# Performance work log

Hardware: AMD Instinct MI355X
Metric: run time of the kernel (lower is better)

## Reference

```python
import jax, jax.numpy as jnp
import numpy as np

D_MODEL = 1024
NUM_HEADS = 16
HEAD_DIM = D_MODEL // NUM_HEADS


def setup_inputs() -> dict:
    key = jax.random.key(0)
    ks = jax.random.split(key, 6)
    B, S = 2, 2048
    s = 1.0 / np.sqrt(D_MODEL)
    return {
        "x": jax.random.normal(ks[0], (B, S, D_MODEL), dtype=jnp.float32),
        "Wq": jax.random.normal(ks[1], (D_MODEL, D_MODEL), dtype=jnp.float32) * s,
        "Wk": jax.random.normal(ks[2], (D_MODEL, D_MODEL), dtype=jnp.float32) * s,
        "Wv": jax.random.normal(ks[3], (D_MODEL, D_MODEL), dtype=jnp.float32) * s,
        "Wo": jax.random.normal(ks[4], (D_MODEL, D_MODEL), dtype=jnp.float32) * s,
        "bo": jax.random.normal(ks[5], (D_MODEL,), dtype=jnp.float32) * 0.01,
    }


def reference(x, Wq, Wk, Wv, Wo, bo):
    b, n, _ = x.shape
    # QKV projections (no bias, qkv_bias=False); weights applied as x @ W^T like nn.Linear
    q = (x @ Wq.T).reshape(b, n, NUM_HEADS, HEAD_DIM).transpose(0, 2, 1, 3)  # [b,h,n,d]
    k = (x @ Wk.T).reshape(b, n, NUM_HEADS, HEAD_DIM).transpose(0, 2, 1, 3)
    v = (x @ Wv.T).reshape(b, n, NUM_HEADS, HEAD_DIM).transpose(0, 2, 1, 3)
    scores = jnp.einsum("bhqd,bhkd->bhqk", q, k)
    causal = jnp.tril(jnp.ones((n, n), dtype=bool))  # keep where True
    scores = jnp.where(causal, scores, -jnp.inf)
    weights = jax.nn.softmax(scores / np.sqrt(HEAD_DIM), axis=-1)
    # dropout p=0.0 -> identity (eval semantics)
    ctx = jnp.einsum("bhqk,bhkd->bhqd", weights, v)
    ctx = ctx.transpose(0, 2, 1, 3).reshape(b, n, D_MODEL)
    return ctx @ Wo.T + bo
```

## Files before the change

### kernel.cpp

```cpp
#include <hip/hip_runtime.h>

#define D_MODEL 1024
#define NUM_HEADS 16
#define HEAD_DIM 64
#define BATCH 2
#define SEQ 2048
#define MTOT (BATCH * SEQ)

typedef __attribute__((ext_vector_type(8))) short bf16x8;
typedef __attribute__((ext_vector_type(4))) short s16x4;
typedef __attribute__((ext_vector_type(4))) float f32x4;
typedef unsigned short u16;
typedef unsigned long long u64;

__device__ __forceinline__ u16 f2bf(float f) {
    unsigned u = __float_as_uint(f);
    return (u16)((u + 0x7FFFu + ((u >> 16) & 1u)) >> 16);
}
__device__ __forceinline__ float bf2f(u16 v) {
    return __uint_as_float((unsigned)v << 16);
}

__device__ __forceinline__ unsigned cvt_pk_bf16(float lo, float hi) {
    unsigned r;
    asm volatile("v_cvt_pk_bf16_f32 %0, %1, %2" : "=v"(r) : "v"(lo), "v"(hi));
    return r;
}

#if __has_builtin(__builtin_amdgcn_exp2f)
#define EXP2(x) __builtin_amdgcn_exp2f(x)
#else
#define EXP2(x) exp2f(x)
#endif

#define GLOAD16(gp, lp) __builtin_amdgcn_global_load_lds(                      \
    (const __attribute__((address_space(1))) void*)(gp),                       \
    (__attribute__((address_space(3))) void*)(lp), 16, 0, 0)

__global__ __launch_bounds__(256)
void cast_all_kernel(const float* __restrict__ x,  const float* __restrict__ Wq,
                     const float* __restrict__ Wk, const float* __restrict__ Wv,
                     const float* __restrict__ Wo, u16* __restrict__ dst)
{
    const int i = blockIdx.x * 256 + threadIdx.x;
    const float* src;
    int j;
    if (i < 524288) { src = x; j = i; }
    else if (i < 917504) {
        const int k = i - 524288;
        const int z = k >> 17;
        src = (z == 0) ? Wq : (z == 1) ? Wk : Wv;
        j = k & 0x1FFFF;
    } else { src = Wo; j = i - 917504; }
    const float4* s = reinterpret_cast<const float4*>(src) + (size_t)j * 2;
    float4 a = s[0], b = s[1];
    u16 tmp[8] = {f2bf(a.x), f2bf(a.y), f2bf(a.z), f2bf(a.w),
                  f2bf(b.x), f2bf(b.y), f2bf(b.z), f2bf(b.w)};
    *reinterpret_cast<int4*>(dst + (size_t)i * 8) = *reinterpret_cast<int4*>(tmp);
}

__global__ __launch_bounds__(512, 4)
void gemm_qkv_kernel(const u16* __restrict__ A, const u16* __restrict__ B,
                     u16* __restrict__ Qo, u16* __restrict__ Ko, u16* __restrict__ Vt)
{
    __shared__ u16 Al[3][128 * 32];
    __shared__ u16 Bl[3][256 * 32];

    const int tid = threadIdx.x;
    const int l = tid & 63;
    const int w = tid >> 6;
    const int wm = w >> 2, wn = w & 3;
    const int lr = l & 15, lg = l >> 4;

    const int bid = blockIdx.x;
    const int swz = (bid & 7) * 48 + (bid >> 3);
    const int mb = swz / 12, nb = swz % 12;
    const int m0 = mb * 128, n0 = nb * 256;

    const int arow = tid >> 2;
    const int acol = ((tid & 3) ^ ((arow >> 1) & 3)) * 8;
    const int br1  = (512 + tid) >> 2;
    const int bcol1 = ((tid & 3) ^ ((br1 >> 1) & 3)) * 8;
    const int dst0 = tid * 8;
    const int dst1 = 4096 + tid * 8;
    const int rsw = (lr >> 1) & 3;

    f32x4 acc[4][4];
    #pragma unroll
    for (int i = 0; i < 4; ++i)
        #pragma unroll
        for (int j = 0; j < 4; ++j) acc[i][j] = (f32x4){0.f, 0.f, 0.f, 0.f};

    #pragma unroll
    for (int t = 0; t < 2; ++t) {
        const int k0 = t * 32;
        GLOAD16(A + (size_t)(m0 + arow) * D_MODEL + k0 + acol,  &Al[t][dst0]);
        GLOAD16(B + (size_t)(n0 + arow) * D_MODEL + k0 + acol,  &Bl[t][dst0]);
        GLOAD16(B + (size_t)(n0 + br1)  * D_MODEL + k0 + bcol1, &Bl[t][dst1]);
    }

    int cb = 0;
    for (int t = 0; t < 32; ++t) {
        if (t < 31) asm volatile("s_waitcnt vmcnt(3)" ::: "memory");
        else        asm volatile("s_waitcnt vmcnt(0)" ::: "memory");
        __builtin_amdgcn_s_barrier();

        if (t + 2 < 32) {
            const int sb = (cb >= 1) ? cb - 1 : cb + 2;
            const int k0 = (t + 2) * 32;
            GLOAD16(A + (size_t)(m0 + arow) * D_MODEL + k0 + acol,  &Al[sb][dst0]);
            GLOAD16(B + (size_t)(n0 + arow) * D_MODEL + k0 + acol,  &Bl[sb][dst0]);
            GLOAD16(B + (size_t)(n0 + br1)  * D_MODEL + k0 + bcol1, &Bl[sb][dst1]);
        }

        const u16* __restrict__ Ab = Al[cb];
        const u16* __restrict__ Bb = Bl[cb];
        bf16x8 af[4], bfr[4];
        #pragma unroll
        for (int i = 0; i < 4; ++i)
            af[i] = *reinterpret_cast<const bf16x8*>(
                &Ab[(wm * 64 + i * 16 + lr) * 32 + ((lg ^ rsw) * 8)]);
        #pragma unroll
        for (int j = 0; j < 4; ++j)
            bfr[j] = *reinterpret_cast<const bf16x8*>(
                &Bb[(wn * 64 + j * 16 + lr) * 32 + ((lg ^ rsw) * 8)]);

        __builtin_amdgcn_s_setprio(1);
        #pragma unroll
        for (int i = 0; i < 4; ++i)
            #pragma unroll
            for (int j = 0; j < 4; ++j)
                acc[i][j] = __builtin_amdgcn_mfma_f32_16x16x32_bf16(
                    af[i], bfr[j], acc[i][j], 0, 0, 0);
        __builtin_amdgcn_s_setprio(0);

        cb = (cb == 2) ? 0 : cb + 1;
    }

    const int z = (n0 >> 10);
    if (z < 2) {
        #pragma unroll
        for (int i = 0; i < 4; ++i) {
            #pragma unroll
            for (int r = 0; r < 4; ++r) {
                const int m = m0 + wm * 64 + i * 16 + lg * 4 + r;
                const int bb = m >> 11, s = m & (SEQ - 1);
                #pragma unroll
                for (int j = 0; j < 4; ++j) {
                    const int c = n0 + wn * 64 + j * 16 + lr;
                    const int cc = c & 1023, h = cc >> 6, d = cc & 63;
                    const size_t idx = ((size_t)(bb * NUM_HEADS + h) * SEQ + s) * 64 + d;
                    if (z == 0) Qo[idx] = f2bf(acc[i][j][r] * 0.18033688f);
                    else        Ko[idx] = f2bf(acc[i][j][r]);
                }
            }
        }
    } else {
        #pragma unroll
        for (int i = 0; i < 4; ++i) {
            const int mbase = m0 + wm * 64 + i * 16 + lg * 4;
            const int bb = mbase >> 11, s = mbase & (SEQ - 1);
            #pragma unroll
            for (int j = 0; j < 4; ++j) {
                const int c = n0 + wn * 64 + j * 16 + lr;
                const int cc = c & 1023, h = cc >> 6, d = cc & 63;
                u16 t4[4];
                #pragma unroll
                for (int r = 0; r < 4; ++r) t4[r] = f2bf(acc[i][j][r]);
                *reinterpret_cast<u64*>(
                    &Vt[((size_t)(bb * NUM_HEADS + h) * 64 + d) * SEQ + s]) =
                    *reinterpret_cast<u64*>(t4);
            }
        }
    }
}

__global__ __launch_bounds__(256, 3)
void gemm_out_kernel(const u16* __restrict__ A, const u16* __restrict__ B,
                     const float* __restrict__ bias, float* __restrict__ out)
{
    __shared__ u16 Al[3][128 * 32];
    __shared__ u16 Bl[3][128 * 32];

    const int tid = threadIdx.x;
    const int l = tid & 63;
    const int w = tid >> 6;
    const int wm = w >> 1, wn = w & 1;
    const int lr = l & 15, lg = l >> 4;

    const int bid = blockIdx.x;
    const int swz = (bid & 7) * 32 + (bid >> 3);
    const int mb = swz >> 3, nb = swz & 7;
    const int m0 = mb * 128, n0 = nb * 128;

    const int r0 = tid >> 2;
    const int c0 = ((tid & 3) ^ ((r0 >> 1) & 3)) * 8;
    const int r1 = 64 + (tid >> 2);
    const int c1 = ((tid & 3) ^ ((r1 >> 1) & 3)) * 8;
    const int dst0 = tid * 8;
    const int dst1 = 2048 + tid * 8;
    const int rsw = (lr >> 1) & 3;

    f32x4 acc[4][4];
    #pragma unroll
    for (int i = 0; i < 4; ++i)
        #pragma unroll
        for (int j = 0; j < 4; ++j) acc[i][j] = (f32x4){0.f, 0.f, 0.f, 0.f};

    #pragma unroll
    for (int t = 0; t < 2; ++t) {
        const int k0 = t * 32;
        GLOAD16(A + (size_t)(m0 + r0) * D_MODEL + k0 + c0, &Al[t][dst0]);
        GLOAD16(A + (size_t)(m0 + r1) * D_MODEL + k0 + c1, &Al[t][dst1]);
        GLOAD16(B + (size_t)(n0 + r0) * D_MODEL + k0 + c0, &Bl[t][dst0]);
        GLOAD16(B + (size_t)(n0 + r1) * D_MODEL + k0 + c1, &Bl[t][dst1]);
    }

    int cb = 0;
    for (int t = 0; t < 32; ++t) {
        if (t < 31) asm volatile("s_waitcnt vmcnt(4)" ::: "memory");
        else        asm volatile("s_waitcnt vmcnt(0)" ::: "memory");
        __builtin_amdgcn_s_barrier();

        if (t + 2 < 32) {
            const int sb = (cb >= 1) ? cb - 1 : cb + 2;
            const int k0 = (t + 2) * 32;
            GLOAD16(A + (size_t)(m0 + r0) * D_MODEL + k0 + c0, &Al[sb][dst0]);
            GLOAD16(A + (size_t)(m0 + r1) * D_MODEL + k0 + c1, &Al[sb][dst1]);
            GLOAD16(B + (size_t)(n0 + r0) * D_MODEL + k0 + c0, &Bl[sb][dst0]);
            GLOAD16(B + (size_t)(n0 + r1) * D_MODEL + k0 + c1, &Bl[sb][dst1]);
        }

        const u16* __restrict__ Ab = Al[cb];
        const u16* __restrict__ Bb = Bl[cb];
        bf16x8 af[4], bfr[4];
        #pragma unroll
        for (int i = 0; i < 4; ++i)
            af[i] = *reinterpret_cast<const bf16x8*>(
                &Ab[(wm * 64 + i * 16 + lr) * 32 + ((lg ^ rsw) * 8)]);
        #pragma unroll
        for (int j = 0; j < 4; ++j)
            bfr[j] = *reinterpret_cast<const bf16x8*>(
                &Bb[(wn * 64 + j * 16 + lr) * 32 + ((lg ^ rsw) * 8)]);

        __builtin_amdgcn_s_setprio(1);
        #pragma unroll
        for (int i = 0; i < 4; ++i)
            #pragma unroll
            for (int j = 0; j < 4; ++j)
                acc[i][j] = __builtin_amdgcn_mfma_f32_16x16x32_bf16(
                    af[i], bfr[j], acc[i][j], 0, 0, 0);
        __builtin_amdgcn_s_setprio(0);

        cb = (cb == 2) ? 0 : cb + 1;
    }

    #pragma unroll
    for (int i = 0; i < 4; ++i) {
        #pragma unroll
        for (int r = 0; r < 4; ++r) {
            const int m = m0 + wm * 64 + i * 16 + lg * 4 + r;
            #pragma unroll
            for (int j = 0; j < 4; ++j) {
                const int c = n0 + wn * 64 + j * 16 + lr;
                out[(size_t)m * D_MODEL + c] = acc[i][j][r] + bias[c];
            }
        }
    }
}

__device__ __forceinline__ void map_pair128(int p, int& qt2, int& ch) {
    if (p < 16)      { qt2 = 15 - (p >> 2); ch = p & 3; }
    else if (p < 28) { int t = p - 16; qt2 = 11 - t / 3; ch = t % 3; }
    else if (p < 36) { int t = p - 28; qt2 = 7 - (t >> 1); ch = t & 1; }
    else             { qt2 = 39 - p; ch = 0; }
}

__global__ __launch_bounds__(256)
void attn_kernel(const u16* __restrict__ Q, const u16* __restrict__ K,
                 const u16* __restrict__ Vt, u16* __restrict__ ctx,
                 u16* __restrict__ Opart, float* __restrict__ Lpart)
{
    __shared__ char LdsB[2][16384];

    const int tid = threadIdx.x;
    const int l = tid & 63;
    const int w = tid >> 6;
    const int lr = l & 15;
    const int lg = l >> 4;

    const int xcd  = blockIdx.x & 7;
    const int slot = blockIdx.x >> 3;
    const int bh   = xcd * 4 + slot / 40;
    int qt2, ch;
    map_pair128(slot % 40, qt2, ch);

    const int ntiles = 2 * qt2 + 2;
    const int nch  = (ntiles + 7) >> 3;
    const int base = ntiles / nch, rem = ntiles % nch;
    const int start = ch * base + (ch < rem ? ch : rem);
    const int cnt   = base + (ch < rem ? 1 : 0);

    const size_t hbase = (size_t)bh * SEQ * 64;
    const int b = bh >> 4, h = bh & (NUM_HEADS - 1);
    const u16* __restrict__ Kh = K + hbase;
    const u16* __restrict__ Vh = Vt + hbase;
    const int q0 = qt2 * 128;

    const int r0 = tid >> 3;
    const int c0 = ((tid & 7) ^ (r0 & 7)) * 8;
    const int r1 = (256 + tid) >> 3;
    const int c1 = ((tid & 7) ^ (r1 & 7)) * 8;
    const int d0b = tid * 16;
    const int d1b = 4096 + tid * 16;
    const int rswz = (lr & 7) << 4;

    bf16x8 qf[2][2];
    #pragma unroll
    for (int fq = 0; fq < 2; ++fq) {
        const u16* qp = Q + hbase + (size_t)(q0 + fq * 64 + w * 16 + lr) * 64 + lg * 8;
        qf[fq][0] = *reinterpret_cast<const bf16x8*>(qp);
        qf[fq][1] = *reinterpret_cast<const bf16x8*>(qp + 32);
    }
    asm volatile("s_waitcnt vmcnt(0)" ::: "memory");

    f32x4 acc[2][4];
    #pragma unroll
    for (int fq = 0; fq < 2; ++fq)
        #pragma unroll
        for (int nb = 0; nb < 4; ++nb) acc[fq][nb] = (f32x4){0.f, 0.f, 0.f, 0.f};
    float lsumv[2] = {0.f, 0.f};

    {
        char* kb = LdsB[0];
        char* vb = LdsB[0] + 8192;
        const int kb64 = start * 64;
        GLOAD16(Kh + (size_t)(kb64 + r0) * 64 + c0, kb + d0b);
        GLOAD16(Kh + (size_t)(kb64 + r1) * 64 + c1, kb + d1b);
        GLOAD16(Vh + (size_t)r0 * SEQ + kb64 + c0, vb + d0b);
        GLOAD16(Vh + (size_t)r1 * SEQ + kb64 + c1, vb + d1b);
    }

    for (int it = 0; it < cnt; ++it) {
        const int tile = start + it;
        const int buf = it & 1;

        asm volatile("s_waitcnt vmcnt(0)" ::: "memory");
        __builtin_amdgcn_s_barrier();

        if (it < cnt - 1) {
            const int kb64 = (tile + 1) * 64;
            char* kbl = LdsB[buf ^ 1];
            char* vbl = kbl + 8192;
            GLOAD16(Kh + (size_t)(kb64 + r0) * 64 + c0, kbl + d0b);
            GLOAD16(Kh + (size_t)(kb64 + r1) * 64 + c1, kbl + d1b);
            GLOAD16(Vh + (size_t)r0 * SEQ + kb64 + c0, vbl + d0b);
            GLOAD16(Vh + (size_t)r1 * SEQ + kb64 + c1, vbl + d1b);
        }

        const char* kbuf = LdsB[buf];
        const char* vbuf = kbuf + 8192;

        bf16x8 kf[4][2];
        #pragma unroll
        for (int m = 0; m < 4; ++m) {
            const char* krow = kbuf + (16 * m + lr) * 128;
            kf[m][0] = *reinterpret_cast<const bf16x8*>(krow + ((lg * 16) ^ rswz));
            kf[m][1] = *reinterpret_cast<const bf16x8*>(krow + ((64 + lg * 16) ^ rswz));
        }

        const bool diag = (tile >= 2 * qt2);
        const int koff0 = (tile - 2 * qt2) * 64;

        unsigned dw[2][4][2];
        __builtin_amdgcn_s_setprio(1);
        #pragma unroll
        for (int fq = 0; fq < 2; ++fq) {
            f32x4 s[4];
            #pragma unroll
            for (int m = 0; m < 4; ++m) {
                s[m] = (f32x4){0.f, 0.f, 0.f, 0.f};
                s[m] = __builtin_amdgcn_mfma_f32_16x16x32_bf16(kf[m][0], qf[fq][0], s[m], 0, 0, 0);
                s[m] = __builtin_amdgcn_mfma_f32_16x16x32_bf16(kf[m][1], qf[fq][1], s[m], 0, 0, 0);
            }
            if (diag) {
                const int qloc = fq * 64 + w * 16 + lr;
                #pragma unroll
                for (int m = 0; m < 4; ++m)
                    #pragma unroll
                    for (int r = 0; r < 4; ++r)
                        if (koff0 + 16 * m + 4 * lg + r > qloc) s[m][r] = -1.0e38f;
            }
            float p[4][4];
            #pragma unroll
            for (int m = 0; m < 4; ++m) {
                #pragma unroll
                for (int r = 0; r < 4; ++r) p[m][r] = EXP2(s[m][r]);
                lsumv[fq] += (p[m][0] + p[m][1]) + (p[m][2] + p[m][3]);
                dw[fq][m][0] = cvt_pk_bf16(p[m][0], p[m][1]);
                dw[fq][m][1] = cvt_pk_bf16(p[m][2], p[m][3]);
            }
        }

        #pragma unroll
        for (int c = 0; c < 2; ++c) {
            union Pu { unsigned u[4]; bf16x8 v; } pb[2];
            #pragma unroll
            for (int fq = 0; fq < 2; ++fq) {
                pb[fq].u[0] = dw[fq][2 * c][0];     pb[fq].u[1] = dw[fq][2 * c][1];
                pb[fq].u[2] = dw[fq][2 * c + 1][0]; pb[fq].u[3] = dw[fq][2 * c + 1][1];
            }
            #pragma unroll
            for (int nb = 0; nb < 4; ++nb) {
                const char* vrow = vbuf + (16 * nb + lr) * 128;
                union Vu { s16x4 hv[2]; bf16x8 v; } vf;
                vf.hv[0] = *reinterpret_cast<const s16x4*>(
                    vrow + ((c * 64 + lg * 8) ^ rswz));
                vf.hv[1] = *reinterpret_cast<const s16x4*>(
                    vrow + ((c * 64 + 32 + lg * 8) ^ rswz));
                acc[0][nb] = __builtin_amdgcn_mfma_f32_16x16x32_bf16(
                    vf.v, pb[0].v, acc[0][nb], 0, 0, 0);
                acc[1][nb] = __builtin_amdgcn_mfma_f32_16x16x32_bf16(
                    vf.v, pb[1].v, acc[1][nb], 0, 0, 0);
            }
        }
        __builtin_amdgcn_s_setprio(0);
    }

    #pragma unroll
    for (int fq = 0; fq < 2; ++fq) {
        lsumv[fq] += __shfl_xor(lsumv[fq], 16);
        lsumv[fq] += __shfl_xor(lsumv[fq], 32);
    }

    if (nch == 1) {
        #pragma unroll
        for (int fq = 0; fq < 2; ++fq) {
            const float inv = 1.0f / lsumv[fq];
            const int qrow = q0 + fq * 64 + w * 16 + lr;
            u16* op = ctx + ((size_t)(b * SEQ) + qrow) * D_MODEL + h * 64 + 4 * lg;
            #pragma unroll
            for (int nb = 0; nb < 4; ++nb) {
                u16 t4[4];
                #pragma unroll
                for (int r = 0; r < 4; ++r) t4[r] = f2bf(acc[fq][nb][r] * inv);
                *reinterpret_cast<u64*>(op + 16 * nb) = *reinterpret_cast<u64*>(t4);
            }
        }
    } else {
        const int slot4 = ((bh * 12 + (qt2 - 4)) << 2) + ch;
        #pragma unroll
        for (int fq = 0; fq < 2; ++fq) {
            const int rloc = fq * 64 + w * 16 + lr;
            u16* op = Opart + (size_t)slot4 * 8192 + rloc * 64 + 4 * lg;
            #pragma unroll
            for (int nb = 0; nb < 4; ++nb) {
                u16 t4[4];
                #pragma unroll
                for (int r = 0; r < 4; ++r) t4[r] = f2bf(acc[fq][nb][r]);
                *reinterpret_cast<u64*>(op + 16 * nb) = *reinterpret_cast<u64*>(t4);
            }
            if (lg == 0) Lpart[slot4 * 128 + rloc] = lsumv[fq];
        }
    }
}

__global__ __launch_bounds__(128)
void attn_reduce_kernel(const u16* __restrict__ Opart,
                        const float* __restrict__ Lpart,
                        u16* __restrict__ ctx)
{
    const int blk = blockIdx.x;
    const int bh = blk / 12, idx = blk % 12;
    const int qt2 = idx + 4;
    const int nch = (2 * qt2 + 2 + 7) >> 3;
    const int t = threadIdx.x;
    const int b = bh >> 4, h = bh & (NUM_HEADS - 1);
    const int slot0 = (bh * 12 + idx) << 2;

    float acc[64] = {};
    float lt = 0.f;
    for (int ch = 0; ch < nch; ++ch) {
        const u16* op = Opart + (size_t)(slot0 + ch) * 8192 + t * 64;
        lt += Lpart[(slot0 + ch) * 128 + t];
        #pragma unroll
        for (int cchunk = 0; cchunk < 8; ++cchunk) {
            u16 v[8];
            *reinterpret_cast<int4*>(v) =
                *reinterpret_cast<const int4*>(op + cchunk * 8);
            #pragma unroll
            for (int j = 0; j < 8; ++j) acc[cchunk * 8 + j] += bf2f(v[j]);
        }
    }
    const float inv = 1.0f / lt;
    u16* orow = ctx + ((size_t)(b * SEQ) + qt2 * 128 + t) * D_MODEL + h * 64;
    #pragma unroll
    for (int cchunk = 0; cchunk < 8; ++cchunk) {
        u16 v[8];
        #pragma unroll
        for (int j = 0; j < 8; ++j) v[j] = f2bf(acc[cchunk * 8 + j] * inv);
        *reinterpret_cast<int4*>(orow + cchunk * 8) = *reinterpret_cast<int4*>(v);
    }
}


extern "C" void kernel_launch(void* const* d_in, const int* in_sizes, int n_in,
                              void* d_out, int out_size, void* d_ws, size_t ws_size,
                              hipStream_t stream)
{
    const float* x  = (const float*)d_in[0];
    const float* Wq = (const float*)d_in[1];
    const float* Wk = (const float*)d_in[2];
    const float* Wv = (const float*)d_in[3];
    const float* Wo = (const float*)d_in[4];
    const float* bo = (const float*)d_in[5];
    float* out = (float*)d_out;

    u16* xb   = (u16*)d_ws;
    u16* wqkv = xb   + (size_t)MTOT * D_MODEL;
    u16* wob  = wqkv + (size_t)3 * D_MODEL * D_MODEL;
    u16* Qw   = wob  + (size_t)D_MODEL * D_MODEL;
    u16* Kw   = Qw   + (size_t)MTOT * D_MODEL;
    u16* Vtw  = Kw   + (size_t)MTOT * D_MODEL;
    u16* ctxb = Vtw  + (size_t)MTOT * D_MODEL;
    u16* Opart = ctxb + (size_t)MTOT * D_MODEL;
    float* Lpart = (float*)(Opart + (size_t)1536 * 8192);

    cast_all_kernel<<<4096, 256, 0, stream>>>(x, Wq, Wk, Wv, Wo, xb);

    gemm_qkv_kernel<<<dim3(384), 512, 0, stream>>>(xb, wqkv, Qw, Kw, Vtw);

    attn_kernel<<<dim3(1280), 256, 0, stream>>>(Qw, Kw, Vtw, ctxb, Opart, Lpart);
    attn_reduce_kernel<<<dim3(384), 128, 0, stream>>>(Opart, Lpart, ctxb);

    dim3 go(D_MODEL / 128, MTOT / 128);
    gemm_out_kernel<<<go.x * go.y, 256, 0, stream>>>(ctxb, wob, bo, out);
}
```

Baseline: 117.1 us.

## Double attention query tile to 256 rows with 512-thread blocks

The attention kernel now processes 256-query tiles per block with 8 waves instead of 128-query tiles with 4 waves. Each K/V tile loaded into LDS is shared by twice as many queries, and each thread issues half as many global-to-LDS loads. The chunk mapping, partial-output layout and reduce kernel are resized to match, halving the grid sizes. The trade-off is fewer blocks, which may hurt load balance and occupancy, and more masked work on diagonal tiles.

```diff
diff --git a/kernel.cpp b/kernel.cpp
--- a/kernel.cpp
+++ b/kernel.cpp
@@ -269,14 +269,14 @@
     }
 }
 
-__device__ __forceinline__ void map_pair128(int p, int& qt2, int& ch) {
-    if (p < 16)      { qt2 = 15 - (p >> 2); ch = p & 3; }
-    else if (p < 28) { int t = p - 16; qt2 = 11 - t / 3; ch = t % 3; }
-    else if (p < 36) { int t = p - 28; qt2 = 7 - (t >> 1); ch = t & 1; }
-    else             { qt2 = 39 - p; ch = 0; }
-}
-
-__global__ __launch_bounds__(256)
+__device__ __forceinline__ void map_pair20(int p, int& qt4, int& ch) {
+    if (p < 8)       { qt4 = 7 - (p >> 2); ch = p & 3; }
+    else if (p < 14) { int t = p - 8;  qt4 = 5 - t / 3;   ch = t % 3; }
+    else if (p < 18) { int t = p - 14; qt4 = 3 - (t >> 1); ch = t & 1; }
+    else             { qt4 = 19 - p; ch = 0; }
+}
+
+__global__ __launch_bounds__(512)
 void attn_kernel(const u16* __restrict__ Q, const u16* __restrict__ K,
                  const u16* __restrict__ Vt, u16* __restrict__ ctx,
                  u16* __restrict__ Opart, float* __restrict__ Lpart)
@@ -291,11 +291,11 @@
 
     const int xcd  = blockIdx.x & 7;
     const int slot = blockIdx.x >> 3;
-    const int bh   = xcd * 4 + slot / 40;
-    int qt2, ch;
-    map_pair128(slot % 40, qt2, ch);
-
-    const int ntiles = 2 * qt2 + 2;
+    const int bh   = xcd * 4 + slot / 20;
+    int qt4, ch;
+    map_pair20(slot % 20, qt4, ch);
+
+    const int ntiles = 4 * qt4 + 4;
     const int nch  = (ntiles + 7) >> 3;
     const int base = ntiles / nch, rem = ntiles % nch;
     const int start = ch * base + (ch < rem ? ch : rem);
@@ -305,20 +305,17 @@
     const int b = bh >> 4, h = bh & (NUM_HEADS - 1);
     const u16* __restrict__ Kh = K + hbase;
     const u16* __restrict__ Vh = Vt + hbase;
-    const int q0 = qt2 * 128;
-
-    const int r0 = tid >> 3;
-    const int c0 = ((tid & 7) ^ (r0 & 7)) * 8;
-    const int r1 = (256 + tid) >> 3;
-    const int c1 = ((tid & 7) ^ (r1 & 7)) * 8;
-    const int d0b = tid * 16;
-    const int d1b = 4096 + tid * 16;
+    const int q0 = qt4 * 256;
+
+    const int kr = tid >> 3;
+    const int kc = ((tid & 7) ^ (kr & 7)) * 8;
+    const int dstb = tid * 16;
     const int rswz = (lr & 7) << 4;
 
     bf16x8 qf[2][2];
     #pragma unroll
     for (int fq = 0; fq < 2; ++fq) {
-        const u16* qp = Q + hbase + (size_t)(q0 + fq * 64 + w * 16 + lr) * 64 + lg * 8;
+        const u16* qp = Q + hbase + (size_t)(q0 + fq * 128 + w * 16 + lr) * 64 + lg * 8;
         qf[fq][0] = *reinterpret_cast<const bf16x8*>(qp);
         qf[fq][1] = *reinterpret_cast<const bf16x8*>(qp + 32);
     }
@@ -332,13 +329,9 @@
     float lsumv[2] = {0.f, 0.f};
 
     {
-        char* kb = LdsB[0];
-        char* vb = LdsB[0] + 8192;
         const int kb64 = start * 64;
-        GLOAD16(Kh + (size_t)(kb64 + r0) * 64 + c0, kb + d0b);
-        GLOAD16(Kh + (size_t)(kb64 + r1) * 64 + c1, kb + d1b);
-        GLOAD16(Vh + (size_t)r0 * SEQ + kb64 + c0, vb + d0b);
-        GLOAD16(Vh + (size_t)r1 * SEQ + kb64 + c1, vb + d1b);
+        GLOAD16(Kh + (size_t)(kb64 + kr) * 64 + kc, LdsB[0] + dstb);
+        GLOAD16(Vh + (size_t)kr * SEQ + kb64 + kc, LdsB[0] + 8192 + dstb);
     }
 
     for (int it = 0; it < cnt; ++it) {
@@ -351,11 +344,8 @@
         if (it < cnt - 1) {
             const int kb64 = (tile + 1) * 64;
             char* kbl = LdsB[buf ^ 1];
-            char* vbl = kbl + 8192;
-            GLOAD16(Kh + (size_t)(kb64 + r0) * 64 + c0, kbl + d0b);
-            GLOAD16(Kh + (size_t)(kb64 + r1) * 64 + c1, kbl + d1b);
-            GLOAD16(Vh + (size_t)r0 * SEQ + kb64 + c0, vbl + d0b);
-            GLOAD16(Vh + (size_t)r1 * SEQ + kb64 + c1, vbl + d1b);
+            GLOAD16(Kh + (size_t)(kb64 + kr) * 64 + kc, kbl + dstb);
+            GLOAD16(Vh + (size_t)kr * SEQ + kb64 + kc, kbl + 8192 + dstb);
         }
 
         const char* kbuf = LdsB[buf];
@@ -369,8 +359,8 @@
             kf[m][1] = *reinterpret_cast<const bf16x8*>(krow + ((64 + lg * 16) ^ rswz));
         }
 
-        const bool diag = (tile >= 2 * qt2);
-        const int koff0 = (tile - 2 * qt2) * 64;
+        const bool diag = (tile >= 4 * qt4);
+        const int koff0 = (tile - 4 * qt4) * 64;
 
         unsigned dw[2][4][2];
         __builtin_amdgcn_s_setprio(1);
@@ -384,7 +374,7 @@
                 s[m] = __builtin_amdgcn_mfma_f32_16x16x32_bf16(kf[m][1], qf[fq][1], s[m], 0, 0, 0);
             }
             if (diag) {
-                const int qloc = fq * 64 + w * 16 + lr;
+                const int qloc = fq * 128 + w * 16 + lr;
                 #pragma unroll
                 for (int m = 0; m < 4; ++m)
                     #pragma unroll
@@ -437,7 +427,7 @@
         #pragma unroll
         for (int fq = 0; fq < 2; ++fq) {
             const float inv = 1.0f / lsumv[fq];
-            const int qrow = q0 + fq * 64 + w * 16 + lr;
+            const int qrow = q0 + fq * 128 + w * 16 + lr;
             u16* op = ctx + ((size_t)(b * SEQ) + qrow) * D_MODEL + h * 64 + 4 * lg;
             #pragma unroll
             for (int nb = 0; nb < 4; ++nb) {
@@ -448,11 +438,11 @@
             }
         }
     } else {
-        const int slot4 = ((bh * 12 + (qt2 - 4)) << 2) + ch;
+        const int slot4 = ((bh * 6 + (qt4 - 2)) << 2) + ch;
         #pragma unroll
         for (int fq = 0; fq < 2; ++fq) {
-            const int rloc = fq * 64 + w * 16 + lr;
-            u16* op = Opart + (size_t)slot4 * 8192 + rloc * 64 + 4 * lg;
+            const int rloc = fq * 128 + w * 16 + lr;
+            u16* op = Opart + (size_t)slot4 * 16384 + rloc * 64 + 4 * lg;
             #pragma unroll
             for (int nb = 0; nb < 4; ++nb) {
                 u16 t4[4];
@@ -460,29 +450,29 @@
                 for (int r = 0; r < 4; ++r) t4[r] = f2bf(acc[fq][nb][r]);
                 *reinterpret_cast<u64*>(op + 16 * nb) = *reinterpret_cast<u64*>(t4);
             }
-            if (lg == 0) Lpart[slot4 * 128 + rloc] = lsumv[fq];
-        }
-    }
-}
-
-__global__ __launch_bounds__(128)
+            if (lg == 0) Lpart[slot4 * 256 + rloc] = lsumv[fq];
+        }
+    }
+}
+
+__global__ __launch_bounds__(256)
 void attn_reduce_kernel(const u16* __restrict__ Opart,
                         const float* __restrict__ Lpart,
                         u16* __restrict__ ctx)
 {
     const int blk = blockIdx.x;
-    const int bh = blk / 12, idx = blk % 12;
-    const int qt2 = idx + 4;
-    const int nch = (2 * qt2 + 2 + 7) >> 3;
+    const int bh = blk / 6, idx = blk % 6;
+    const int qt4 = idx + 2;
+    const int nch = (4 * qt4 + 11) >> 3;
     const int t = threadIdx.x;
     const int b = bh >> 4, h = bh & (NUM_HEADS - 1);
-    const int slot0 = (bh * 12 + idx) << 2;
+    const int slot0 = (bh * 6 + idx) << 2;
 
     float acc[64] = {};
     float lt = 0.f;
     for (int ch = 0; ch < nch; ++ch) {
-        const u16* op = Opart + (size_t)(slot0 + ch) * 8192 + t * 64;
-        lt += Lpart[(slot0 + ch) * 128 + t];
+        const u16* op = Opart + (size_t)(slot0 + ch) * 16384 + t * 64;
+        lt += Lpart[(slot0 + ch) * 256 + t];
         #pragma unroll
         for (int cchunk = 0; cchunk < 8; ++cchunk) {
             u16 v[8];
@@ -493,7 +483,7 @@
         }
     }
     const float inv = 1.0f / lt;
-    u16* orow = ctx + ((size_t)(b * SEQ) + qt2 * 128 + t) * D_MODEL + h * 64;
+    u16* orow = ctx + ((size_t)(b * SEQ) + qt4 * 256 + t) * D_MODEL + h * 64;
     #pragma unroll
     for (int cchunk = 0; cchunk < 8; ++cchunk) {
         u16 v[8];
@@ -524,15 +514,14 @@
     u16* Vtw  = Kw   + (size_t)MTOT * D_MODEL;
     u16* ctxb = Vtw  + (size_t)MTOT * D_MODEL;
     u16* Opart = ctxb + (size_t)MTOT * D_MODEL;
-    float* Lpart = (float*)(Opart + (size_t)1536 * 8192);
+    float* Lpart = (float*)(Opart + (size_t)768 * 16384);
 
     cast_all_kernel<<<4096, 256, 0, stream>>>(x, Wq, Wk, Wv, Wo, xb);
 
     gemm_qkv_kernel<<<dim3(384), 512, 0, stream>>>(xb, wqkv, Qw, Kw, Vtw);
 
-    attn_kernel<<<dim3(1280), 256, 0, stream>>>(Qw, Kw, Vtw, ctxb, Opart, Lpart);
-    attn_reduce_kernel<<<dim3(384), 128, 0, stream>>>(Opart, Lpart, ctxb);
-
-    dim3 go(D_MODEL / 128, MTOT / 128);
-    gemm_out_kernel<<<go.x * go.y, 256, 0, stream>>>(ctxb, wob, bo, out);
-}
+    attn_kernel<<<dim3(640), 512, 0, stream>>>(Qw, Kw, Vtw, ctxb, Opart, Lpart);
+    attn_reduce_kernel<<<dim3(192), 256, 0, stream>>>(Opart, Lpart, ctxb);
+
+    gemm_out_kernel<<<dim3(256), 256, 0, stream>>>(ctxb, wob, bo, out);
+}
```

Result: slower. 121.3 us (+3.6%).
